# Performance work log

Hardware: AMD Instinct MI355X
Metric: run time of the kernel (lower is better)

## Reference

```python
import jax, jax.numpy as jnp
import numpy as np

N = 100000   # num nodes
E = 800000   # num edges (random-walk metapath graph)
IN = 256     # in_size
H = 8        # layer_num_heads
D = 32       # out_size per head
HD = H * D   # 256, semantic attention in_size
HID = 128    # semantic attention hidden
NEG_SLOPE = 0.2  # DGL GATConv leaky_relu slope


def setup_inputs() -> dict:
    key = jax.random.key(0)
    ks = jax.random.split(key, 10)
    h = jax.random.normal(ks[0], (N, IN), dtype=jnp.float32)
    src = jax.random.randint(ks[1], (E,), 0, N)
    dst = jax.random.randint(ks[2], (E,), 0, N)
    s = 0.05
    W_fc = jax.random.normal(ks[3], (IN, HD), dtype=jnp.float32) * s
    attn_l = jax.random.normal(ks[4], (H, D), dtype=jnp.float32) * s
    attn_r = jax.random.normal(ks[5], (H, D), dtype=jnp.float32) * s
    bias = jnp.zeros((HD,), dtype=jnp.float32)
    sem_W1 = jax.random.normal(ks[6], (HD, HID), dtype=jnp.float32) * s
    sem_b1 = jnp.zeros((HID,), dtype=jnp.float32)
    sem_W2 = jax.random.normal(ks[7], (HID, 1), dtype=jnp.float32) * s
    return {"h": h, "W_fc": W_fc, "attn_l": attn_l, "attn_r": attn_r,
            "bias": bias, "sem_W1": sem_W1, "sem_b1": sem_b1,
            "sem_W2": sem_W2, "src": src, "dst": dst}


def _gat(h, W_fc, attn_l, attn_r, bias, src, dst):
    feat = (h @ W_fc).reshape(N, H, D)                      # [N,H,D]
    el = jnp.sum(feat * attn_l, axis=-1)                    # [N,H]
    er = jnp.sum(feat * attn_r, axis=-1)                    # [N,H]
    e = jax.nn.leaky_relu(el[src] + er[dst], NEG_SLOPE)     # [E,H]
    # edge softmax over incoming edges per destination node
    mx = jax.ops.segment_max(e, dst, num_segments=N)        # [N,H], -inf for isolated
    mx = jnp.where(jnp.isfinite(mx), mx, 0.0)
    ee = jnp.exp(e - mx[dst])                               # [E,H]
    denom = jax.ops.segment_sum(ee, dst, num_segments=N)    # [N,H]
    alpha = ee / denom[dst]                                 # [E,H]
    msg = feat[src] * alpha[:, :, None]                     # [E,H,D] gather+weight
    rst = jax.ops.segment_sum(msg, dst, num_segments=N)     # [N,H,D] scatter-add
    rst = rst + bias.reshape(H, D)
    return jax.nn.elu(rst).reshape(N, HD)                   # activation=F.elu, flatten(1)


def reference(h, W_fc, attn_l, attn_r, bias, sem_W1, sem_b1, sem_W2, src, dst):
    out = _gat(h, W_fc, attn_l, attn_r, bias, src, dst)     # [N, HD]
    z = out[:, None, :]                                     # [N, 1, HD] single metapath
    w = (jnp.tanh(z @ sem_W1 + sem_b1) @ sem_W2).mean(0)    # [1, 1]
    beta = jax.nn.softmax(w, axis=0)                        # [1, 1]
    return jnp.sum(beta * z, axis=1)                        # [N, HD]
```

## Files before the change

kernel.cpp:

```cpp
#include <hip/hip_runtime.h>
#include <math.h>


#define NN 100000
#define NE 800000

typedef __attribute__((ext_vector_type(8))) short bf16x8;
typedef __attribute__((ext_vector_type(4))) float f32x4;

__device__ __forceinline__ unsigned short f2b(float f){
  unsigned u = __float_as_uint(f);
  return (unsigned short)((u + 0x7FFFu + ((u >> 16) & 1u)) >> 16);
}
__device__ __forceinline__ float b2f(unsigned short b){
  return __uint_as_float(((unsigned)b) << 16);
}

__global__ void k_init(int* __restrict__ cnt, int* __restrict__ cur){
  int i = blockIdx.x * 256 + threadIdx.x;
  if (i < NN){ cnt[i] = 0; cur[i] = 0; }
}

__global__ void k_prep(const float* __restrict__ W, unsigned short* __restrict__ Wt){
  int i = blockIdx.x * 256 + threadIdx.x;
  int n = i >> 8, k = i & 255;
  Wt[n * 256 + k] = f2b(W[k * 256 + n]);
}

__global__ __launch_bounds__(256) void k_gemm(const float* __restrict__ A,
    const unsigned short* __restrict__ Wt, unsigned short* __restrict__ feat){
  __shared__ unsigned short lA[64][40];
  __shared__ unsigned short lB[256][40];
  const int t = threadIdx.x;
  const int lane = t & 63;
  const int wave = t >> 6;
  const int wm = wave >> 1, wn = wave & 1;
  const int bm = blockIdx.x * 64;
  const int l15 = lane & 15, lg = lane >> 4;

  f32x4 acc[2][8];
  #pragma unroll
  for (int i = 0; i < 2; ++i)
    #pragma unroll
    for (int j = 0; j < 8; ++j){ f32x4 z = {0.f,0.f,0.f,0.f}; acc[i][j] = z; }

  const int arow = t >> 2, ac8 = (t & 3) * 8;

  for (int kt = 0; kt < 8; ++kt){
    float4 a0 = {0,0,0,0}, a1 = {0,0,0,0};
    int gr = bm + arow;
    if (gr < NN){
      const float* p = A + (size_t)gr * 256 + kt * 32 + ac8;
      a0 = *(const float4*)p;
      a1 = *(const float4*)(p + 4);
    }
    uint4 bw[4];
    #pragma unroll
    for (int i = 0; i < 4; ++i){
      int c = i * 256 + t;
      bw[i] = *(const uint4*)(Wt + (c >> 2) * 256 + kt * 32 + (c & 3) * 8);
    }
    __syncthreads();
    {
      uint4 av;
      av.x = (unsigned)f2b(a0.x) | ((unsigned)f2b(a0.y) << 16);
      av.y = (unsigned)f2b(a0.z) | ((unsigned)f2b(a0.w) << 16);
      av.z = (unsigned)f2b(a1.x) | ((unsigned)f2b(a1.y) << 16);
      av.w = (unsigned)f2b(a1.z) | ((unsigned)f2b(a1.w) << 16);
      *(uint4*)&lA[arow][ac8] = av;
      #pragma unroll
      for (int i = 0; i < 4; ++i){
        int c = i * 256 + t;
        *(uint4*)&lB[c >> 2][(c & 3) * 8] = bw[i];
      }
    }
    __syncthreads();
    bf16x8 af0 = *(const bf16x8*)&lA[wm * 32 + l15][lg * 8];
    bf16x8 af1 = *(const bf16x8*)&lA[wm * 32 + 16 + l15][lg * 8];
    #pragma unroll
    for (int ni = 0; ni < 8; ++ni){
      bf16x8 bf = *(const bf16x8*)&lB[wn * 128 + ni * 16 + l15][lg * 8];
      acc[0][ni] = __builtin_amdgcn_mfma_f32_16x16x32_bf16(af0, bf, acc[0][ni], 0, 0, 0);
      acc[1][ni] = __builtin_amdgcn_mfma_f32_16x16x32_bf16(af1, bf, acc[1][ni], 0, 0, 0);
    }
  }
  #pragma unroll
  for (int mi = 0; mi < 2; ++mi){
    #pragma unroll
    for (int ni = 0; ni < 8; ++ni){
      int c = wn * 128 + ni * 16 + l15;
      int r0 = bm + wm * 32 + mi * 16 + lg * 4;
      #pragma unroll
      for (int reg = 0; reg < 4; ++reg){
        int r = r0 + reg;
        if (r < NN) feat[(size_t)r * 256 + c] = f2b(acc[mi][ni][reg]);
      }
    }
  }
}

__global__ void k_elr(const unsigned short* __restrict__ feat,
                      const float* __restrict__ attn_l, const float* __restrict__ attn_r,
                      float* __restrict__ el, float* __restrict__ er){
  int i = blockIdx.x * 256 + threadIdx.x;
  if (i >= NN * 8) return;
  int h = i & 7;
  const unsigned short* f = feat + (size_t)i * 32;
  const float* al = attn_l + h * 32;
  const float* ar = attn_r + h * 32;
  float sl = 0.f, sr = 0.f;
  #pragma unroll
  for (int j = 0; j < 4; ++j){
    uint4 v = *(const uint4*)(f + j * 8);
    unsigned vv[4] = {v.x, v.y, v.z, v.w};
    #pragma unroll
    for (int q = 0; q < 4; ++q){
      float x0 = b2f((unsigned short)(vv[q] & 0xffffu));
      float x1 = b2f((unsigned short)(vv[q] >> 16));
      int d = j * 8 + q * 2;
      sl += x0 * al[d] + x1 * al[d + 1];
      sr += x0 * ar[d] + x1 * ar[d + 1];
    }
  }
  el[i] = sl; er[i] = sr;
}

__global__ void k_edge1(const int* __restrict__ dst, int* __restrict__ cnt){
  int e = blockIdx.x * 256 + threadIdx.x;
  if (e < NE) atomicAdd(&cnt[dst[e]], 1);
}

__global__ __launch_bounds__(1024) void k_scanA(const int* __restrict__ cnt,
    int* __restrict__ partial, int* __restrict__ bsum){
  __shared__ int lds[1024];
  int t = threadIdx.x;
  int i = blockIdx.x * 1024 + t;
  int v = (i < NN) ? cnt[i] : 0;
  lds[t] = v;
  __syncthreads();
  for (int off = 1; off < 1024; off <<= 1){
    int add = (t >= off) ? lds[t - off] : 0;
    __syncthreads();
    lds[t] += add;
    __syncthreads();
  }
  if (i < NN) partial[i] = lds[t] - v;
  if (t == 1023) bsum[blockIdx.x] = lds[1023];
}

__global__ void k_scanB(const int* __restrict__ bsum, int* __restrict__ boff, int nb){
  if (threadIdx.x == 0 && blockIdx.x == 0){
    int run = 0;
    for (int i = 0; i < nb; ++i){ boff[i] = run; run += bsum[i]; }
  }
}

__global__ void k_edge2(const int* __restrict__ src, const int* __restrict__ dst,
                        const int* __restrict__ partial, const int* __restrict__ boff,
                        int* __restrict__ cur, int* __restrict__ csr_src){
  int e = blockIdx.x * 256 + threadIdx.x;
  if (e >= NE) return;
  int s = src[e], d = dst[e];
  int slot = partial[d] + boff[d >> 10] + atomicAdd(&cur[d], 1);
  csr_src[slot] = s;
}

__global__ __launch_bounds__(256) void k_agg(const int* __restrict__ csr_src,
    const float* __restrict__ el, const float* __restrict__ er,
    const unsigned short* __restrict__ feat, const int* __restrict__ partial,
    const int* __restrict__ boff, const float* __restrict__ bias, float* __restrict__ out){
  int n = blockIdx.x * 4 + (threadIdx.x >> 6);
  if (n >= NN) return;
  int t = threadIdx.x & 63;
  int h = t >> 3;
  int beg = partial[n] + boff[n >> 10];
  int end = (n + 1 < NN) ? (partial[n + 1] + boff[(n + 1) >> 10]) : NE;
  float ern = er[(size_t)n * 8 + h];
  float den = 0.f, a0 = 0.f, a1 = 0.f, a2 = 0.f, a3 = 0.f;
  for (int i = beg; i < end; ++i){
    int s = csr_src[i];
    float e = el[(size_t)s * 8 + h] + ern;
    float x = e > 0.f ? e : 0.2f * e;
    float ee = __expf(x);
    den += ee;
    uint2 fv = *(const uint2*)(feat + (size_t)s * 256 + t * 4);
    a0 += ee * b2f((unsigned short)(fv.x & 0xffffu));
    a1 += ee * b2f((unsigned short)(fv.x >> 16));
    a2 += ee * b2f((unsigned short)(fv.y & 0xffffu));
    a3 += ee * b2f((unsigned short)(fv.y >> 16));
  }
  float inv = den > 0.f ? 1.f / den : 0.f;
  const float* bp = bias + t * 4;
  float4 o; float x;
  x = a0 * inv + bp[0]; o.x = x > 0.f ? x : expm1f(x);
  x = a1 * inv + bp[1]; o.y = x > 0.f ? x : expm1f(x);
  x = a2 * inv + bp[2]; o.z = x > 0.f ? x : expm1f(x);
  x = a3 * inv + bp[3]; o.w = x > 0.f ? x : expm1f(x);
  *(float4*)(out + (size_t)n * 256 + t * 4) = o;
}

extern "C" void kernel_launch(void* const* d_in, const int* in_sizes, int n_in,
                              void* d_out, int out_size, void* d_ws, size_t ws_size,
                              hipStream_t stream){
  (void)in_sizes; (void)n_in; (void)out_size; (void)ws_size;
  const float* h      = (const float*)d_in[0];
  const float* W_fc   = (const float*)d_in[1];
  const float* attn_l = (const float*)d_in[2];
  const float* attn_r = (const float*)d_in[3];
  const float* bias   = (const float*)d_in[4];
  const int* src = (const int*)d_in[8];
  const int* dst = (const int*)d_in[9];
  float* out = (float*)d_out;

  char* w = (char*)d_ws;
  auto alloc = [&](size_t b){ char* p = w; w += (b + 255) & ~(size_t)255; return p; };
  unsigned short* feat = (unsigned short*)alloc((size_t)NN * 256 * 2);
  unsigned short* Wt   = (unsigned short*)alloc(256 * 256 * 2);
  float* el      = (float*)alloc((size_t)NN * 8 * 4);
  float* er      = (float*)alloc((size_t)NN * 8 * 4);
  int*   cnt     = (int*)alloc((size_t)NN * 4);
  int*   cur     = (int*)alloc((size_t)NN * 4);
  int*   partial = (int*)alloc((size_t)NN * 4);
  int*   bsum    = (int*)alloc(128 * 4);
  int*   boff    = (int*)alloc(128 * 4);
  int*   csr_src = (int*)alloc((size_t)NE * 4);

  const int nb = (NN + 1023) / 1024;

  k_init <<<(NN + 255) / 256, 256, 0, stream>>>(cnt, cur);
  k_prep <<<(256 * 256) / 256, 256, 0, stream>>>(W_fc, Wt);
  k_gemm <<<(NN + 63) / 64, 256, 0, stream>>>(h, Wt, feat);
  k_elr  <<<(NN * 8 + 255) / 256, 256, 0, stream>>>(feat, attn_l, attn_r, el, er);
  k_edge1<<<(NE + 255) / 256, 256, 0, stream>>>(dst, cnt);
  k_scanA<<<nb, 1024, 0, stream>>>(cnt, partial, bsum);
  k_scanB<<<1, 64, 0, stream>>>(bsum, boff, nb);
  k_edge2<<<(NE + 255) / 256, 256, 0, stream>>>(src, dst, partial, boff, cur, csr_src);
  k_agg  <<<(NN + 3) / 4, 256, 0, stream>>>(csr_src, el, er, feat, partial, boff, bias, out);
}
```

Before: 500.1 us.

## Prefetch GEMM tiles, widen aggregation loads, parallelize scan, merge init kernels

The GEMM now issues the global loads for the next K tile right after the LDS barrier, so they overlap the MFMA work on the current tile. The aggregation kernel splits each wave into two halves that handle alternating edges with 16-byte feature loads and reduce across halves with a shuffle. This gives more memory-level parallelism per edge and fewer load instructions. The serial block-offset scan becomes a parallel LDS scan, and the init and weight-prep kernels are merged to save a launch, at the cost of more registers in the GEMM.

Measured after the change: 466.0 us. -6.8%, faster.

```diff
diff --git a/kernel.cpp b/kernel.cpp
--- a/kernel.cpp
+++ b/kernel.cpp
@@ -16,15 +16,11 @@
   return __uint_as_float(((unsigned)b) << 16);
 }
 
-__global__ void k_init(int* __restrict__ cnt, int* __restrict__ cur){
+__global__ void k_prep(const float* __restrict__ W, unsigned short* __restrict__ Wt,
+                       int* __restrict__ cnt, int* __restrict__ cur){
   int i = blockIdx.x * 256 + threadIdx.x;
+  if (i < 65536){ int n = i >> 8, k = i & 255; Wt[n * 256 + k] = f2b(W[k * 256 + n]); }
   if (i < NN){ cnt[i] = 0; cur[i] = 0; }
-}
-
-__global__ void k_prep(const float* __restrict__ W, unsigned short* __restrict__ Wt){
-  int i = blockIdx.x * 256 + threadIdx.x;
-  int n = i >> 8, k = i & 255;
-  Wt[n * 256 + k] = f2b(W[k * 256 + n]);
 }
 
 __global__ __launch_bounds__(256) void k_gemm(const float* __restrict__ A,
@@ -45,21 +41,24 @@
     for (int j = 0; j < 8; ++j){ f32x4 z = {0.f,0.f,0.f,0.f}; acc[i][j] = z; }
 
   const int arow = t >> 2, ac8 = (t & 3) * 8;
-
+  const int gr = bm + arow;
+
+  float4 a0, a1; uint4 bw[4];
+#define LOADG(KT) do {                                                        \
+    float4 z4 = {0.f,0.f,0.f,0.f}; a0 = z4; a1 = z4;                          \
+    if (gr < NN){                                                             \
+      const float* p = A + (size_t)gr * 256 + (KT) * 32 + ac8;                \
+      a0 = *(const float4*)p; a1 = *(const float4*)(p + 4);                   \
+    }                                                                         \
+    _Pragma("unroll")                                                         \
+    for (int i_ = 0; i_ < 4; ++i_){                                           \
+      int c = i_ * 256 + t;                                                   \
+      bw[i_] = *(const uint4*)(Wt + (size_t)(c >> 2) * 256 + (KT) * 32 + (c & 3) * 8); \
+    }                                                                         \
+  } while (0)
+
+  LOADG(0);
   for (int kt = 0; kt < 8; ++kt){
-    float4 a0 = {0,0,0,0}, a1 = {0,0,0,0};
-    int gr = bm + arow;
-    if (gr < NN){
-      const float* p = A + (size_t)gr * 256 + kt * 32 + ac8;
-      a0 = *(const float4*)p;
-      a1 = *(const float4*)(p + 4);
-    }
-    uint4 bw[4];
-    #pragma unroll
-    for (int i = 0; i < 4; ++i){
-      int c = i * 256 + t;
-      bw[i] = *(const uint4*)(Wt + (c >> 2) * 256 + kt * 32 + (c & 3) * 8);
-    }
     __syncthreads();
     {
       uint4 av;
@@ -75,6 +74,7 @@
       }
     }
     __syncthreads();
+    if (kt < 7) LOADG(kt + 1);
     bf16x8 af0 = *(const bf16x8*)&lA[wm * 32 + l15][lg * 8];
     bf16x8 af1 = *(const bf16x8*)&lA[wm * 32 + 16 + l15][lg * 8];
     #pragma unroll
@@ -84,6 +84,7 @@
       acc[1][ni] = __builtin_amdgcn_mfma_f32_16x16x32_bf16(af1, bf, acc[1][ni], 0, 0, 0);
     }
   }
+#undef LOADG
   #pragma unroll
   for (int mi = 0; mi < 2; ++mi){
     #pragma unroll
@@ -148,11 +149,20 @@
   if (t == 1023) bsum[blockIdx.x] = lds[1023];
 }
 
-__global__ void k_scanB(const int* __restrict__ bsum, int* __restrict__ boff, int nb){
-  if (threadIdx.x == 0 && blockIdx.x == 0){
-    int run = 0;
-    for (int i = 0; i < nb; ++i){ boff[i] = run; run += bsum[i]; }
-  }
+__global__ __launch_bounds__(128) void k_scanB(const int* __restrict__ bsum,
+                                               int* __restrict__ boff, int nb){
+  __shared__ int lds[128];
+  int t = threadIdx.x;
+  int v = (t < nb) ? bsum[t] : 0;
+  lds[t] = v;
+  __syncthreads();
+  for (int off = 1; off < 128; off <<= 1){
+    int add = (t >= off) ? lds[t - off] : 0;
+    __syncthreads();
+    lds[t] += add;
+    __syncthreads();
+  }
+  if (t < nb) boff[t] = lds[t] - v;
 }
 
 __global__ void k_edge2(const int* __restrict__ src, const int* __restrict__ dst,
@@ -165,38 +175,70 @@
   csr_src[slot] = s;
 }
 
+__device__ __forceinline__ void acc8(float* a, uint4 f, float w){
+  unsigned u[4] = {f.x, f.y, f.z, f.w};
+  #pragma unroll
+  for (int j = 0; j < 4; ++j){
+    a[2 * j]     += w * __uint_as_float(u[j] << 16);
+    a[2 * j + 1] += w * __uint_as_float(u[j] & 0xffff0000u);
+  }
+}
+
 __global__ __launch_bounds__(256) void k_agg(const int* __restrict__ csr_src,
     const float* __restrict__ el, const float* __restrict__ er,
     const unsigned short* __restrict__ feat, const int* __restrict__ partial,
     const int* __restrict__ boff, const float* __restrict__ bias, float* __restrict__ out){
   int n = blockIdx.x * 4 + (threadIdx.x >> 6);
   if (n >= NN) return;
-  int t = threadIdx.x & 63;
-  int h = t >> 3;
+  const int t = threadIdx.x & 63;
+  const int half = t >> 5;
+  const int q = t & 31;
+  const int h = q >> 2;
   int beg = partial[n] + boff[n >> 10];
   int end = (n + 1 < NN) ? (partial[n + 1] + boff[(n + 1) >> 10]) : NE;
   float ern = er[(size_t)n * 8 + h];
-  float den = 0.f, a0 = 0.f, a1 = 0.f, a2 = 0.f, a3 = 0.f;
-  for (int i = beg; i < end; ++i){
-    int s = csr_src[i];
-    float e = el[(size_t)s * 8 + h] + ern;
-    float x = e > 0.f ? e : 0.2f * e;
-    float ee = __expf(x);
-    den += ee;
-    uint2 fv = *(const uint2*)(feat + (size_t)s * 256 + t * 4);
-    a0 += ee * b2f((unsigned short)(fv.x & 0xffffu));
-    a1 += ee * b2f((unsigned short)(fv.x >> 16));
-    a2 += ee * b2f((unsigned short)(fv.y & 0xffffu));
-    a3 += ee * b2f((unsigned short)(fv.y >> 16));
-  }
+  float den = 0.f;
+  float a[8] = {0.f,0.f,0.f,0.f,0.f,0.f,0.f,0.f};
+  const unsigned short* fb = feat + q * 8;
+
+  int i = beg;
+  for (; i + 4 <= end; i += 4){
+    int s0 = csr_src[i + half];
+    int s1 = csr_src[i + 2 + half];
+    uint4 f0 = *(const uint4*)(fb + (size_t)s0 * 256);
+    uint4 f1 = *(const uint4*)(fb + (size_t)s1 * 256);
+    float e0 = el[(size_t)s0 * 8 + h] + ern;
+    float e1 = el[(size_t)s1 * 8 + h] + ern;
+    e0 = e0 > 0.f ? e0 : 0.2f * e0;  e0 = __expf(e0);
+    e1 = e1 > 0.f ? e1 : 0.2f * e1;  e1 = __expf(e1);
+    den += e0 + e1;
+    acc8(a, f0, e0);
+    acc8(a, f1, e1);
+  }
+  for (; i < end; i += 2){
+    int ia = i + half;
+    if (ia < end){
+      int s = csr_src[ia];
+      uint4 f = *(const uint4*)(fb + (size_t)s * 256);
+      float e = el[(size_t)s * 8 + h] + ern;
+      e = e > 0.f ? e : 0.2f * e;  e = __expf(e);
+      den += e;
+      acc8(a, f, e);
+    }
+  }
+  den += __shfl_xor(den, 32);
+  #pragma unroll
+  for (int j = 0; j < 8; ++j) a[j] += __shfl_xor(a[j], 32);
   float inv = den > 0.f ? 1.f / den : 0.f;
-  const float* bp = bias + t * 4;
-  float4 o; float x;
-  x = a0 * inv + bp[0]; o.x = x > 0.f ? x : expm1f(x);
-  x = a1 * inv + bp[1]; o.y = x > 0.f ? x : expm1f(x);
-  x = a2 * inv + bp[2]; o.z = x > 0.f ? x : expm1f(x);
-  x = a3 * inv + bp[3]; o.w = x > 0.f ? x : expm1f(x);
-  *(float4*)(out + (size_t)n * 256 + t * 4) = o;
+
+  const float* bp = bias + q * 8 + half * 4;
+  float4 o;
+  #pragma unroll
+  for (int j = 0; j < 4; ++j){
+    float v = (half ? a[4 + j] : a[j]) * inv + bp[j];
+    ((float*)&o)[j] = v > 0.f ? v : expm1f(v);
+  }
+  *(float4*)(out + (size_t)n * 256 + q * 8 + half * 4) = o;
 }
 
 extern "C" void kernel_launch(void* const* d_in, const int* in_sizes, int n_in,
@@ -227,13 +269,12 @@
 
   const int nb = (NN + 1023) / 1024;
 
-  k_init <<<(NN + 255) / 256, 256, 0, stream>>>(cnt, cur);
-  k_prep <<<(256 * 256) / 256, 256, 0, stream>>>(W_fc, Wt);
+  k_prep <<<(NN + 255) / 256, 256, 0, stream>>>(W_fc, Wt, cnt, cur);
   k_gemm <<<(NN + 63) / 64, 256, 0, stream>>>(h, Wt, feat);
   k_elr  <<<(NN * 8 + 255) / 256, 256, 0, stream>>>(feat, attn_l, attn_r, el, er);
   k_edge1<<<(NE + 255) / 256, 256, 0, stream>>>(dst, cnt);
   k_scanA<<<nb, 1024, 0, stream>>>(cnt, partial, bsum);
-  k_scanB<<<1, 64, 0, stream>>>(bsum, boff, nb);
+  k_scanB<<<1, 128, 0, stream>>>(bsum, boff, nb);
   k_edge2<<<(NE + 255) / 256, 256, 0, stream>>>(src, dst, partial, boff, cur, csr_src);
   k_agg  <<<(NN + 3) / 4, 256, 0, stream>>>(csr_src, el, er, feat, partial, boff, bias, out);
 }
```
